# Optimization experiments

Hardware: AMD Instinct MI355X
Metric: run time of the kernel (lower is better)

## Reference

```python
import jax, jax.numpy as jnp
import numpy as np

N_NODES = 100000
N_EDGES = 3200000


def setup_inputs() -> dict:
    key = jax.random.key(0)
    ks = jax.random.split(key, 12)
    x = jax.random.normal(ks[0], (N_NODES, 5), dtype=jnp.float32)
    edges = jax.random.randint(ks[1], (2, N_EDGES), 0, N_NODES)
    edge_attr = jax.random.normal(ks[2], (N_EDGES, 2), dtype=jnp.float32)
    detector_labels = jax.random.bernoulli(ks[3], 0.7, (N_NODES,))

    def init(k, shape, fan_in):
        return (jax.random.normal(k, shape, dtype=jnp.float32) / np.sqrt(fan_in)).astype(jnp.float32)

    W_gat = init(ks[4], (5, 16), 5)        # GATConv lin (shared src/dst)
    att_src = init(ks[5], (16,), 16)
    att_dst = init(ks[6], (16,), 16)
    W_edge = init(ks[7], (2, 16), 2)       # GATConv lin_edge
    att_edge = init(ks[8], (16,), 16)
    b_gat = jnp.zeros((16,), jnp.float32)
    W1 = init(ks[9], (34, 64), 34)
    b1 = jnp.zeros((64,), jnp.float32)
    W2 = init(ks[10], (64, 2), 64)
    b2 = jnp.zeros((2,), jnp.float32)
    return dict(x=x, edges=edges, edge_attr=edge_attr, detector_labels=detector_labels,
                W_gat=W_gat, att_src=att_src, att_dst=att_dst, W_edge=W_edge,
                att_edge=att_edge, b_gat=b_gat, W1=W1, b1=b1, W2=W2, b2=b2)


def reference(x, edges, edge_attr, detector_labels, W_gat, att_src, att_dst,
              W_edge, att_edge, b_gat, W1, b1, W2, b2):
    n_nodes = x.shape[0]
    src, dst = edges[0], edges[1]

    # --- GATConv(5 -> 16, heads=1, concat=False, edge_dim=2, no self loops) ---
    h = x @ W_gat                                        # [N, 16]
    a_src = h @ att_src                                  # [N]
    a_dst = h @ att_dst                                  # [N]
    a_edge = (edge_attr @ W_edge) @ att_edge             # [E]
    alpha = jax.nn.leaky_relu(a_src[src] + a_dst[dst] + a_edge, 0.2)
    # segmented softmax over incoming edges of each dst node
    seg_max = jax.ops.segment_max(alpha, dst, num_segments=n_nodes)
    ex = jnp.exp(alpha - seg_max[dst])
    denom = jax.ops.segment_sum(ex, dst, num_segments=n_nodes)
    a = ex / (denom[dst] + 1e-16)                        # [E]
    out = jax.ops.segment_sum(h[src] * a[:, None], dst, num_segments=n_nodes) + b_gat
    xh = jax.nn.relu(out)                                # [N, 16]

    # --- edge update: gather-concat-MLP ---
    feat = jnp.concatenate([xh[src], edge_attr, xh[dst]], axis=-1)   # [E, 34]
    ef = jax.nn.relu(feat @ W1 + b1) @ W2 + b2                       # [E, 2]

    # --- SplitSyndromes: keep edges whose both endpoints are detectors ---
    valid = detector_labels[src] & detector_labels[dst]
    idx = jnp.nonzero(valid)[0]        # eager (data-dependent size, not jitted)
    return edges[:, idx], jax.nn.sigmoid(ef[idx])
```

## Files before the change

kernel.cpp:

```cpp
#include <hip/hip_runtime.h>

#define NN 100000
#define NE 3200000
#define CH 8192
#define NCB ((NE + CH - 1) / CH)
#define THR 1024
#define ITH (CH / THR)
#define NBK ((NN + 63) >> 6)
#define CAP 2560
#define NWG (NE / 64)
#define NSTRIP 8
#define SLEN ((NCB + NSTRIP - 1) / NSTRIP)

typedef __attribute__((ext_vector_type(8))) __bf16 bf16x8;
typedef __attribute__((ext_vector_type(4))) float f32x4;

union BF8 { unsigned short u[8]; bf16x8 v; };

__global__ void kdetect(const unsigned char* __restrict__ lab8, int* __restrict__ flags) {
  __shared__ int tmp[256];
  int t = threadIdx.x;
  int s = 0;
  for (int i = t; i < 25000; i += 256) s += lab8[4 * i + 1];
  tmp[t] = s;
  __syncthreads();
  for (int d = 128; d > 0; d >>= 1) { if (t < d) tmp[t] += tmp[t + d]; __syncthreads(); }
  if (t == 0) flags[0] = (tmp[0] != 0) ? 1 : 0;
}

__global__ void klab(const void* __restrict__ lab, const int* __restrict__ flags,
                     int* __restrict__ labN) {
  int n = blockIdx.x * 256 + threadIdx.x;
  if (n >= NN) return;
  int v;
  if (flags[0]) v = ((const unsigned char*)lab)[n];
  else          v = ((const int*)lab)[n];
  labN[n] = (v != 0) ? 1 : 0;
}

__global__ void kc01(const float* __restrict__ We, const float* __restrict__ ae,
                     float* __restrict__ c01) {
  if (threadIdx.x == 0) {
    float c0 = 0.f, c1 = 0.f;
    for (int k = 0; k < 16; k++) { c0 += We[k] * ae[k]; c1 += We[16 + k] * ae[k]; }
    c01[0] = c0; c01[1] = c1;
  }
}

__global__ void knodeA(const float* __restrict__ x, const float* __restrict__ Wg,
                       const float* __restrict__ atts, const float* __restrict__ attd,
                       const int* __restrict__ labN,
                       float2* __restrict__ pka, float2* __restrict__ pkd) {
  int n = blockIdx.x * 256 + threadIdx.x;
  if (n >= NN) return;
  float xi[5];
#pragma unroll
  for (int i = 0; i < 5; i++) xi[i] = x[n * 5 + i];
  float asum = 0.f, dsum = 0.f;
#pragma unroll
  for (int k = 0; k < 16; k++) {
    float acc = 0.f;
#pragma unroll
    for (int i = 0; i < 5; i++) acc += xi[i] * Wg[i * 16 + k];
    asum += acc * atts[k];
    dsum += acc * attd[k];
  }
  float lab = labN[n] ? 1.f : 0.f;
  pka[n] = make_float2(asum, lab);
  pkd[n] = make_float2(dsum, lab);
}

__global__ __launch_bounds__(THR) void khist(const int* __restrict__ src,
                                             const int* __restrict__ dst,
                                             const int* __restrict__ labN,
                                             int* __restrict__ blkcnt,
                                             int* __restrict__ cntw,
                                             int* __restrict__ cntc) {
  __shared__ int hist[NBK];
  __shared__ int vsum;
  int tid = threadIdx.x, b = blockIdx.x;
  for (int i = tid; i < NBK; i += THR) hist[i] = 0;
  if (tid == 0) vsum = 0;
  __syncthreads();
  int lane = tid & 63, wid = tid >> 6;
  int wsum = 0;
  for (int it = 0; it < ITH; ++it) {
    int e = b * CH + it * THR + tid;
    int v = 0;
    if (e < NE) {
      int s = src[e], d = dst[e];
      atomicAdd(&hist[d >> 6], 1);
      v = labN[s] & labN[d];
    }
    unsigned long long m = __ballot(v != 0);
    int c = __popcll(m);
    if (lane == 0) {
      int wg = b * (CH / 64) + it * 16 + wid;
      if (wg < NWG) cntw[wg] = c;
      wsum += c;
    }
  }
  if (lane == 0) atomicAdd(&vsum, wsum);
  __syncthreads();
  int* row = blkcnt + (size_t)b * NBK;
  for (int i = tid; i < NBK; i += THR) row[i] = hist[i];
  if (tid == 0) cntc[b] = vsum;
}

__global__ __launch_bounds__(256) void kscanc1(int* __restrict__ blkcnt,
                                               int* __restrict__ ssum) {
  int i = blockIdx.x * 256 + threadIdx.x;
  int st = blockIdx.y;
  if (i >= NBK) return;
  int c0 = st * SLEN, c1 = min(c0 + SLEN, NCB);
  int run = 0;
  for (int c = c0; c < c1; c++) {
    int* p = blkcnt + (size_t)c * NBK + i;
    int v = *p;
    *p = run;
    run += v;
  }
  ssum[st * NBK + i] = run;
}

__global__ __launch_bounds__(256) void kscanc2(int* __restrict__ ssum,
                                               int* __restrict__ total) {
  int i = blockIdx.x * 256 + threadIdx.x;
  if (i >= NBK) return;
  int run = 0;
#pragma unroll
  for (int st = 0; st < NSTRIP; st++) {
    int v = ssum[st * NBK + i];
    ssum[st * NBK + i] = run;
    run += v;
  }
  total[i] = run;
}

__global__ __launch_bounds__(256) void kaddbb(int* __restrict__ ssum,
                                              const int* __restrict__ bb) {
  int i = blockIdx.x * 256 + threadIdx.x;
  if (i >= NBK) return;
  int v = bb[i];
#pragma unroll
  for (int st = 0; st < NSTRIP; st++) ssum[st * NBK + i] += v;
}

__global__ void kscan(const int* __restrict__ cnt, int* __restrict__ off, int nb) {
  __shared__ int tmp[256];
  __shared__ int carry;
  int t = threadIdx.x;
  if (t == 0) carry = 0;
  __syncthreads();
  for (int base = 0; base < nb; base += 256) {
    int i = base + t;
    int v = (i < nb) ? cnt[i] : 0;
    tmp[t] = v;
    __syncthreads();
    for (int d = 1; d < 256; d <<= 1) {
      int add = (t >= d) ? tmp[t - d] : 0;
      __syncthreads();
      tmp[t] += add;
      __syncthreads();
    }
    if (i < nb) off[i] = carry + tmp[t] - v;
    __syncthreads();
    if (t == 0) carry += tmp[255];
    __syncthreads();
  }
  if (t == 0) off[nb] = carry;
}

__global__ __launch_bounds__(128) void kscanw(const int* __restrict__ cntw,
                                              const int* __restrict__ offc,
                                              int* __restrict__ offw) {
  int b = blockIdx.x, t = threadIdx.x;
  __shared__ int a[128];
  int wg = b * 128 + t;
  int val = (wg < NWG) ? cntw[wg] : 0;
  a[t] = val;
  __syncthreads();
  for (int d = 1; d < 128; d <<= 1) {
    int x = (t >= d) ? a[t - d] : 0;
    __syncthreads();
    a[t] += x;
    __syncthreads();
  }
  if (wg < NWG) offw[wg] = offc[b] + a[t] - val;
}

__device__ __forceinline__ void scat_body(
    int e, int b, int it, int lane, int wid,
    const int* __restrict__ src, const int* __restrict__ dst,
    const float* __restrict__ eattr,
    const float2* __restrict__ pka, const float2* __restrict__ pkd,
    float c0, float c1, int* cur, const int* __restrict__ offw,
    uint2* __restrict__ bins, float* __restrict__ out,
    float2* __restrict__ eat2, int NV) {
  int s = src[e], d = dst[e];
  float2 ea = ((const float2*)eattr)[e];
  float2 ga = pka[s], gd = pkd[d];
  float al = ga.x + gd.x + ea.x * c0 + ea.y * c1;
  al = (al > 0.f) ? al : 0.2f * al;
  float exv = __expf(al);
  int pos = atomicAdd(&cur[d >> 6], 1);
  uint2 pl;
  pl.x = ((unsigned)s << 6) | (unsigned)(d & 63);
  pl.y = __float_as_uint(exv);
  bins[pos] = pl;
  int v = (ga.y != 0.f) && (gd.y != 0.f);
  unsigned long long m = __ballot(v);
  if (v) {
    int wg = b * (CH / 64) + it * 16 + wid;
    int p = offw[wg] + __popcll(m & ((1ull << lane) - 1ull));
    if (p < NV) {
      out[p] = (float)s;
      out[NV + p] = (float)d;
      eat2[p] = ea;
    }
  }
}

__global__ __launch_bounds__(THR) void kscat(
    const int* __restrict__ src, const int* __restrict__ dst,
    const float* __restrict__ eattr,
    const float2* __restrict__ pka, const float2* __restrict__ pkd,
    const float* __restrict__ c01,
    const int* __restrict__ blkcnt, const int* __restrict__ ssum,
    const int* __restrict__ offw,
    uint2* __restrict__ bins, float* __restrict__ out,
    float2* __restrict__ eat2, int NV) {
  __shared__ int cur[NBK];
  int ob = blockIdx.x, tid = threadIdx.x;
  int xcd = ob & 7, loc = ob >> 3;
  const int q = NCB >> 3, r = NCB & 7;
  int b = ((xcd < r) ? xcd * (q + 1) : r * (q + 1) + (xcd - r) * q) + loc;
  const int* bc = blkcnt + (size_t)b * NBK;
  const int* ss = ssum + (size_t)(b / SLEN) * NBK;
  for (int i = tid; i < NBK; i += THR) cur[i] = ss[i] + bc[i];
  float c0 = c01[0], c1 = c01[1];
  __syncthreads();
  int lane = tid & 63, wid = tid >> 6;
  if (b * CH + CH <= NE) {
#pragma unroll
    for (int it = 0; it < ITH; ++it)
      scat_body(b * CH + it * THR + tid, b, it, lane, wid, src, dst, eattr,
                pka, pkd, c0, c1, cur, offw, bins, out, eat2, NV);
  } else {
    for (int it = 0; it < ITH; ++it) {
      int e = b * CH + it * THR + tid;
      if (e >= NE) break;
      scat_body(e, b, it, lane, wid, src, dst, eattr,
                pka, pkd, c0, c1, cur, offw, bins, out, eat2, NV);
    }
  }
}

__global__ __launch_bounds__(512) void kagg(
    const uint2* __restrict__ bins, const int* __restrict__ bucket_base,
    const float* __restrict__ x, const float* __restrict__ Wg,
    const float* __restrict__ bg, float* __restrict__ xh) {
  __shared__ uint2 pay[CAP];
  __shared__ int cnt[64], inc[64], cur[64];
  __shared__ float sWg[80], sbg[16];
  int k = blockIdx.x, tid = threadIdx.x;
  if (tid < 80) sWg[tid] = Wg[tid];
  else if (tid < 96) sbg[tid - 80] = bg[tid - 80];
  int start = bucket_base[k], end = bucket_base[k + 1];
  int node0 = k << 6;
  int c = tid & 15, g = tid >> 4;
  __syncthreads();
  float w0 = sWg[c], w1 = sWg[16 + c], w2 = sWg[32 + c], w3 = sWg[48 + c], w4 = sWg[64 + c];
  float acc[2] = {0.f, 0.f}, den[2] = {0.f, 0.f};
  for (int cb = start; cb < end; cb += CAP) {
    int n = min(end - cb, CAP);
    if (tid < 64) cnt[tid] = 0;
    __syncthreads();
    uint2 st0, st1, st2, st3, st4;
    {
      int i;
      i = tid;          if (i < n) { st0 = bins[cb + i]; atomicAdd(&cnt[st0.x & 63], 1); }
      i = tid + 512;    if (i < n) { st1 = bins[cb + i]; atomicAdd(&cnt[st1.x & 63], 1); }
      i = tid + 1024;   if (i < n) { st2 = bins[cb + i]; atomicAdd(&cnt[st2.x & 63], 1); }
      i = tid + 1536;   if (i < n) { st3 = bins[cb + i]; atomicAdd(&cnt[st3.x & 63], 1); }
      i = tid + 2048;   if (i < n) { st4 = bins[cb + i]; atomicAdd(&cnt[st4.x & 63], 1); }
    }
    __syncthreads();
    if (tid < 64) inc[tid] = cnt[tid];
    __syncthreads();
    for (int d = 1; d < 64; d <<= 1) {
      int v = 0;
      if (tid >= d && tid < 64) v = inc[tid - d];
      __syncthreads();
      if (tid < 64) inc[tid] += v;
      __syncthreads();
    }
    if (tid < 64) cur[tid] = inc[tid] - cnt[tid];
    __syncthreads();
    {
      int i;
      i = tid;          if (i < n) pay[atomicAdd(&cur[st0.x & 63], 1)] = st0;
      i = tid + 512;    if (i < n) pay[atomicAdd(&cur[st1.x & 63], 1)] = st1;
      i = tid + 1024;   if (i < n) pay[atomicAdd(&cur[st2.x & 63], 1)] = st2;
      i = tid + 1536;   if (i < n) pay[atomicAdd(&cur[st3.x & 63], 1)] = st3;
      i = tid + 2048;   if (i < n) pay[atomicAdd(&cur[st4.x & 63], 1)] = st4;
    }
    __syncthreads();
#pragma unroll
    for (int p = 0; p < 2; ++p) {
      int nd = p * 32 + g;
      int re = inc[nd], rs = re - cnt[nd];
      float a = 0.f, ds = 0.f;
      for (int idx = rs; idx < re; ++idx) {
        uint2 pl = pay[idx];
        int s = (int)(pl.x >> 6);
        float exv = __uint_as_float(pl.y);
        const float* xp = x + s * 5;
        float h = xp[0] * w0 + xp[1] * w1 + xp[2] * w2 + xp[3] * w3 + xp[4] * w4;
        a += h * exv;
        ds += exv;
      }
      acc[p] += a; den[p] += ds;
    }
    __syncthreads();
  }
#pragma unroll
  for (int p = 0; p < 2; ++p) {
    int node = node0 + p * 32 + g;
    if (node < NN) {
      float dn = fmaxf(den[p], 1e-30f);
      float v = acc[p] / dn + sbg[c];
      xh[node * 16 + c] = (v > 0.f) ? v : 0.f;
    }
  }
}

__global__ __launch_bounds__(256) void kmlp(
    const float2* __restrict__ eat2, const float* __restrict__ xh,
    const float* __restrict__ W1, const float* __restrict__ b1,
    const float* __restrict__ W2, const float* __restrict__ b2,
    float* __restrict__ out, int NV) {
  int tid = threadIdx.x;
  int lane = tid & 63, wid = tid >> 6;
  int lo4 = lane & 15, q = lane >> 4;

  BF8 bh[4], bl[4];
#pragma unroll
  for (int ct = 0; ct < 4; ct++) {
    int col = ct * 16 + lo4;
#pragma unroll
    for (int i = 0; i < 8; i++) {
      int k = q * 8 + i;
      int r = (k < 16) ? k : (k + 2);
      float w = W1[r * 64 + col];
      unsigned u = __float_as_uint(w);
      float rem = w - __uint_as_float(u & 0xffff0000u);
      bh[ct].u[i] = (unsigned short)(u >> 16);
      bl[ct].u[i] = (unsigned short)(__float_as_uint(rem) >> 16);
    }
  }
  float b1v[4], w16v[4], w17v[4], w2a[4], w2b[4];
#pragma unroll
  for (int ct = 0; ct < 4; ct++) {
    int j = ct * 16 + lo4;
    b1v[ct] = b1[j];
    w16v[ct] = W1[16 * 64 + j];
    w17v[ct] = W1[17 * 64 + j];
    w2a[ct] = W2[j * 2 + 0];
    w2b[ct] = W2[j * 2 + 1];
  }
  float bias20 = b2[0], bias21 = b2[1];

  int nwaves = gridDim.x * 4;
  int ntiles = (NV + 15) >> 4;
  for (int tb = blockIdx.x * 4 + wid; tb < ntiles; tb += nwaves) {
    int base = tb * 16;
    BF8 ah, al;
    {
      int p = base + lo4;
      float vals[8] = {0.f, 0.f, 0.f, 0.f, 0.f, 0.f, 0.f, 0.f};
      if (p < NV) {
        int node = (int)out[((q < 2) ? 0 : NV) + p];
        const float4* xp = (const float4*)(xh + node * 16 + (q & 1) * 8);
        float4 f0 = xp[0], f1 = xp[1];
        vals[0] = f0.x; vals[1] = f0.y; vals[2] = f0.z; vals[3] = f0.w;
        vals[4] = f1.x; vals[5] = f1.y; vals[6] = f1.z; vals[7] = f1.w;
      }
#pragma unroll
      for (int i = 0; i < 8; i++) {
        unsigned u = __float_as_uint(vals[i]);
        float rem = vals[i] - __uint_as_float(u & 0xffff0000u);
        ah.u[i] = (unsigned short)(u >> 16);
        al.u[i] = (unsigned short)(__float_as_uint(rem) >> 16);
      }
    }
    f32x4 acc[4];
#pragma unroll
    for (int ct = 0; ct < 4; ct++) {
      f32x4 z = {0.f, 0.f, 0.f, 0.f};
      z = __builtin_amdgcn_mfma_f32_16x16x32_bf16(ah.v, bh[ct].v, z, 0, 0, 0);
      z = __builtin_amdgcn_mfma_f32_16x16x32_bf16(ah.v, bl[ct].v, z, 0, 0, 0);
      z = __builtin_amdgcn_mfma_f32_16x16x32_bf16(al.v, bh[ct].v, z, 0, 0, 0);
      acc[ct] = z;
    }
    float o0[4], o1[4];
#pragma unroll
    for (int reg = 0; reg < 4; reg++) {
      int pr = base + q * 4 + reg;
      float2 ea = make_float2(0.f, 0.f);
      if (pr < NV) ea = eat2[pr];
      float s0 = 0.f, s1 = 0.f;
#pragma unroll
      for (int ct = 0; ct < 4; ct++) {
        float h = acc[ct][reg] + b1v[ct] + ea.x * w16v[ct] + ea.y * w17v[ct];
        h = fmaxf(h, 0.f);
        s0 += h * w2a[ct];
        s1 += h * w2b[ct];
      }
      o0[reg] = s0; o1[reg] = s1;
    }
#pragma unroll
    for (int m = 1; m < 16; m <<= 1) {
#pragma unroll
      for (int reg = 0; reg < 4; reg++) {
        o0[reg] += __shfl_xor(o0[reg], m, 64);
        o1[reg] += __shfl_xor(o1[reg], m, 64);
      }
    }
    if (lo4 == 0) {
#pragma unroll
      for (int reg = 0; reg < 4; reg++) {
        int pr = base + q * 4 + reg;
        if (pr < NV) {
          float v0 = bias20 + o0[reg], v1 = bias21 + o1[reg];
          ((float2*)(out + 2 * (size_t)NV))[pr] = make_float2(
              1.f / (1.f + __expf(-v0)), 1.f / (1.f + __expf(-v1)));
        }
      }
    }
  }
}

static inline size_t al64(size_t v) { return (v + 63) & ~(size_t)63; }

extern "C" void kernel_launch(void* const* d_in, const int* in_sizes, int n_in,
                              void* d_out, int out_size, void* d_ws, size_t ws_size,
                              hipStream_t stream) {
  const float* x     = (const float*)d_in[0];
  const int*   edges = (const int*)d_in[1];
  const float* eattr = (const float*)d_in[2];
  const void*  labels= d_in[3];
  const float* Wg    = (const float*)d_in[4];
  const float* atts  = (const float*)d_in[5];
  const float* attd  = (const float*)d_in[6];
  const float* We    = (const float*)d_in[7];
  const float* atte  = (const float*)d_in[8];
  const float* bg    = (const float*)d_in[9];
  const float* W1    = (const float*)d_in[10];
  const float* b1    = (const float*)d_in[11];
  const float* W2    = (const float*)d_in[12];
  const float* b2    = (const float*)d_in[13];
  float* out = (float*)d_out;
  const int NV = out_size / 4;
  const int* src = edges;
  const int* dst = edges + NE;

  char* w = (char*)d_ws;
  float* xh    = (float*)w;   w += al64((size_t)NN * 64);
  uint2* bins  = (uint2*)w;   w += al64((size_t)NE * 8);
  float2* eat2 = (float2*)w;  w += al64((size_t)NV * 8);
  float2* pka  = (float2*)w;  w += al64((size_t)NN * 8);
  float2* pkd  = (float2*)w;  w += al64((size_t)NN * 8);
  int* labN    = (int*)w;     w += al64((size_t)NN * 4);
  int* blkcnt  = (int*)w;     w += al64((size_t)NCB * NBK * 4);
  int* ssum    = (int*)w;     w += al64((size_t)NSTRIP * NBK * 4);
  int* total   = (int*)w;     w += al64((size_t)NBK * 4);
  int* bb      = (int*)w;     w += al64((size_t)(NBK + 1) * 4);
  int* cntc    = (int*)w;     w += al64((size_t)NCB * 4);
  int* offc    = (int*)w;     w += al64((size_t)(NCB + 1) * 4);
  int* cntw    = (int*)w;     w += al64((size_t)NWG * 4);
  int* offw    = (int*)w;     w += al64((size_t)NWG * 4);
  float* c01   = (float*)w;   w += 64;
  int* flags   = (int*)w;     w += 64;

  kdetect<<<1, 256, 0, stream>>>((const unsigned char*)labels, flags);
  klab<<<(NN + 255) / 256, 256, 0, stream>>>(labels, flags, labN);
  kc01<<<1, 64, 0, stream>>>(We, atte, c01);
  knodeA<<<(NN + 255) / 256, 256, 0, stream>>>(x, Wg, atts, attd, labN, pka, pkd);
  khist<<<NCB, THR, 0, stream>>>(src, dst, labN, blkcnt, cntw, cntc);
  kscanc1<<<dim3((NBK + 255) / 256, NSTRIP), 256, 0, stream>>>(blkcnt, ssum);
  kscanc2<<<(NBK + 255) / 256, 256, 0, stream>>>(ssum, total);
  kscan<<<1, 256, 0, stream>>>(total, bb, NBK);
  kaddbb<<<(NBK + 255) / 256, 256, 0, stream>>>(ssum, bb);
  kscan<<<1, 256, 0, stream>>>(cntc, offc, NCB);
  kscanw<<<NCB, 128, 0, stream>>>(cntw, offc, offw);
  kscat<<<NCB, THR, 0, stream>>>(src, dst, eattr, pka, pkd, c01, blkcnt, ssum,
                                 offw, bins, out, eat2, NV);
  kagg<<<NBK, 512, 0, stream>>>(bins, bb, x, Wg, bg, xh);
  if (NV > 0)
    kmlp<<<2048, 256, 0, stream>>>(eat2, xh, W1, b1, W2, b2, out, NV);
}
```

Measured before the change: 290.8 us.

## Stage scatter payloads in LDS sorted by bucket before coalesced global write

The scatter kernel now builds a per-block histogram of destination buckets, runs a block-wide prefix scan, and reorders each block's edge payloads in shared memory by bucket. It then writes them to the global bins array contiguously, replacing the random per-edge global stores. This aims to turn scattered 8-byte writes into mostly coalesced runs. The cost is a large LDS footprint (about 100KB, which limits occupancy), extra barriers and scan work, and the removal of the XCD-aware block index remapping.

```diff
diff --git a/kernel.cpp b/kernel.cpp
--- a/kernel.cpp
+++ b/kernel.cpp
@@ -189,38 +189,6 @@
   if (wg < NWG) offw[wg] = offc[b] + a[t] - val;
 }
 
-__device__ __forceinline__ void scat_body(
-    int e, int b, int it, int lane, int wid,
-    const int* __restrict__ src, const int* __restrict__ dst,
-    const float* __restrict__ eattr,
-    const float2* __restrict__ pka, const float2* __restrict__ pkd,
-    float c0, float c1, int* cur, const int* __restrict__ offw,
-    uint2* __restrict__ bins, float* __restrict__ out,
-    float2* __restrict__ eat2, int NV) {
-  int s = src[e], d = dst[e];
-  float2 ea = ((const float2*)eattr)[e];
-  float2 ga = pka[s], gd = pkd[d];
-  float al = ga.x + gd.x + ea.x * c0 + ea.y * c1;
-  al = (al > 0.f) ? al : 0.2f * al;
-  float exv = __expf(al);
-  int pos = atomicAdd(&cur[d >> 6], 1);
-  uint2 pl;
-  pl.x = ((unsigned)s << 6) | (unsigned)(d & 63);
-  pl.y = __float_as_uint(exv);
-  bins[pos] = pl;
-  int v = (ga.y != 0.f) && (gd.y != 0.f);
-  unsigned long long m = __ballot(v);
-  if (v) {
-    int wg = b * (CH / 64) + it * 16 + wid;
-    int p = offw[wg] + __popcll(m & ((1ull << lane) - 1ull));
-    if (p < NV) {
-      out[p] = (float)s;
-      out[NV + p] = (float)d;
-      eat2[p] = ea;
-    }
-  }
-}
-
 __global__ __launch_bounds__(THR) void kscat(
     const int* __restrict__ src, const int* __restrict__ dst,
     const float* __restrict__ eattr,
@@ -230,29 +198,87 @@
     const int* __restrict__ offw,
     uint2* __restrict__ bins, float* __restrict__ out,
     float2* __restrict__ eat2, int NV) {
-  __shared__ int cur[NBK];
-  int ob = blockIdx.x, tid = threadIdx.x;
-  int xcd = ob & 7, loc = ob >> 3;
-  const int q = NCB >> 3, r = NCB & 7;
-  int b = ((xcd < r) ? xcd * (q + 1) : r * (q + 1) + (xcd - r) * q) + loc;
+  __shared__ uint2 pay[CH];
+  __shared__ unsigned short pbk[CH];
+  __shared__ int hist[2048];
+  __shared__ int ps[1024];
+  __shared__ int lcur[2048];
+  __shared__ int goff[NBK];
+  int b = blockIdx.x, tid = threadIdx.x;
+  for (int i = tid; i < 2048; i += THR) hist[i] = 0;
+  float c0 = c01[0], c1 = c01[1];
   const int* bc = blkcnt + (size_t)b * NBK;
   const int* ss = ssum + (size_t)(b / SLEN) * NBK;
-  for (int i = tid; i < NBK; i += THR) cur[i] = ss[i] + bc[i];
-  float c0 = c01[0], c1 = c01[1];
   __syncthreads();
   int lane = tid & 63, wid = tid >> 6;
-  if (b * CH + CH <= NE) {
-#pragma unroll
-    for (int it = 0; it < ITH; ++it)
-      scat_body(b * CH + it * THR + tid, b, it, lane, wid, src, dst, eattr,
-                pka, pkd, c0, c1, cur, offw, bins, out, eat2, NV);
-  } else {
-    for (int it = 0; it < ITH; ++it) {
-      int e = b * CH + it * THR + tid;
-      if (e >= NE) break;
-      scat_body(e, b, it, lane, wid, src, dst, eattr,
-                pka, pkd, c0, c1, cur, offw, bins, out, eat2, NV);
-    }
+  uint2 st[ITH];
+  unsigned short sb[ITH];
+#pragma unroll
+  for (int it = 0; it < ITH; ++it) {
+    int e = b * CH + it * THR + tid;
+    int v = 0;
+    int s = 0, d = 0;
+    float2 ea;
+    if (e < NE) {
+      s = src[e]; d = dst[e];
+      ea = ((const float2*)eattr)[e];
+      float2 ga = pka[s], gd = pkd[d];
+      float al = ga.x + gd.x + ea.x * c0 + ea.y * c1;
+      al = (al > 0.f) ? al : 0.2f * al;
+      float exv = __expf(al);
+      int bk = d >> 6;
+      atomicAdd(&hist[bk], 1);
+      st[it].x = ((unsigned)s << 6) | (unsigned)(d & 63);
+      st[it].y = __float_as_uint(exv);
+      sb[it] = (unsigned short)bk;
+      v = (ga.y != 0.f) && (gd.y != 0.f);
+    } else {
+      sb[it] = 0xffffu;
+    }
+    unsigned long long m = __ballot(v);
+    if (v) {
+      int wg = b * (CH / 64) + it * 16 + wid;
+      int p = offw[wg] + __popcll(m & ((1ull << lane) - 1ull));
+      if (p < NV) {
+        out[p] = (float)s;
+        out[NV + p] = (float)d;
+        eat2[p] = ea;
+      }
+    }
+  }
+  __syncthreads();
+  int h0 = hist[2 * tid], h1 = hist[2 * tid + 1];
+  ps[tid] = h0 + h1;
+  __syncthreads();
+  for (int d = 1; d < 1024; d <<= 1) {
+    int v = (tid >= d) ? ps[tid - d] : 0;
+    __syncthreads();
+    ps[tid] += v;
+    __syncthreads();
+  }
+  int epair = (tid > 0) ? ps[tid - 1] : 0;
+  int l0 = epair, l1 = epair + h0;
+  lcur[2 * tid] = l0;
+  lcur[2 * tid + 1] = l1;
+  {
+    int i0 = 2 * tid, i1 = 2 * tid + 1;
+    if (i0 < NBK) goff[i0] = ss[i0] + bc[i0] - l0;
+    if (i1 < NBK) goff[i1] = ss[i1] + bc[i1] - l1;
+  }
+  __syncthreads();
+#pragma unroll
+  for (int it = 0; it < ITH; ++it) {
+    if (sb[it] != 0xffffu) {
+      int pos = atomicAdd(&lcur[sb[it]], 1);
+      pay[pos] = st[it];
+      pbk[pos] = sb[it];
+    }
+  }
+  __syncthreads();
+  int n = ps[1023];
+  for (int j = tid; j < n; j += THR) {
+    int i = pbk[j];
+    bins[goff[i] + j] = pay[j];
   }
 }
 
```

Result: faster. 280.4 us (-3.6%).
